# Performance work log

Measured on AMD Instinct MI355X. Metric: run time of the kernel, lower is better.

## Reference

```python
import jax, jax.numpy as jnp
import numpy as np

T, B, IN, H, L = 1024, 32, 512, 512, 2


def setup_inputs() -> dict:
    key = jax.random.key(0)
    ks = jax.random.split(key, 9)
    stdv = 1.0 / np.sqrt(H)
    u = lambda k, shape: jax.random.uniform(k, shape, jnp.float32, -stdv, stdv)
    return {
        "x": jax.random.normal(ks[0], (T, B, IN), jnp.float32),
        "w_ih0": u(ks[1], (4 * H, IN)),
        "w_hh0": u(ks[2], (4 * H, H)),
        "b_ih0": jnp.zeros((4 * H,), jnp.float32),
        "b_hh0": jnp.zeros((4 * H,), jnp.float32),
        "w_ih1": u(ks[3], (4 * H, H)),
        "w_hh1": u(ks[4], (4 * H, H)),
        "b_ih1": jnp.zeros((4 * H,), jnp.float32),
        "b_hh1": jnp.zeros((4 * H,), jnp.float32),
        "h0": jnp.zeros((L, B, H), jnp.float32),
        "c0": jnp.zeros((L, B, H), jnp.float32),
    }


def _lstm_layer(x, w_ih, b_ih, w_hh, b_hh, h0, c0):
    # Precompute input projection for the whole sequence (in2hidden), then
    # scan the strictly sequential hidden recurrence over time.
    gi = jnp.einsum("tbi,gi->tbg", x, w_ih) + b_ih  # (T, B, 4H)

    def step(carry, g):
        h, c = carry
        gates = g + h @ w_hh.T + b_hh  # (B, 4H)
        i, f, gcell, o = jnp.split(gates, 4, axis=-1)
        i = jax.nn.sigmoid(i)
        f = jax.nn.sigmoid(f)
        gcell = jnp.tanh(gcell)
        o = jax.nn.sigmoid(o)
        c = f * c + i * gcell
        h = o * jnp.tanh(c)
        return (h, c), h

    (hT, cT), hs = jax.lax.scan(step, (h0, c0), gi)
    return hs, hT, cT  # (T,B,H), (B,H), (B,H)


def reference(x, w_ih0, w_hh0, b_ih0, b_hh0, w_ih1, w_hh1, b_ih1, b_hh1, h0, c0):
    out0, h0f, c0f = _lstm_layer(x, w_ih0, b_ih0, w_hh0, b_hh0, h0[0], c0[0])
    out1, h1f, c1f = _lstm_layer(out0, w_ih1, b_ih1, w_hh1, b_hh1, h0[1], c0[1])
    h_n = jnp.stack([h0f, h1f])  # (L, B, H)
    c_n = jnp.stack([c0f, c1f])
    return out1, h_n, c_n
```

## Files before the change

### kernel.cpp

```cpp
#include <hip/hip_runtime.h>

#define TT 1024
#define BB 32
#define HH 512

typedef __attribute__((ext_vector_type(8))) __bf16 bf16x8;
typedef __attribute__((ext_vector_type(8))) short short8;
typedef __attribute__((ext_vector_type(4))) float f32x4;

union frag_u {
  short8 s;
  bf16x8 b;
  f32x4 f;
  unsigned long long q[2];
  unsigned int d[4];
};

__device__ __forceinline__ unsigned short f2bf(float f) {
  unsigned int u = __float_as_uint(f);
  u += 0x7FFFu + ((u >> 16) & 1u);
  return (unsigned short)(u >> 16);
}

__device__ __forceinline__ bf16x8 cvt8(const float* p) {
  frag_u u;
#pragma unroll
  for (int j = 0; j < 8; ++j) u.s[j] = (short)f2bf(p[j]);
  return u.b;
}

__device__ __forceinline__ float sigm(float x) {
  return __builtin_amdgcn_rcpf(1.0f + __expf(-x));
}
__device__ __forceinline__ float tanh_(float x) {
  return 1.0f - 2.0f * __builtin_amdgcn_rcpf(1.0f + __expf(2.0f * x));
}

__device__ __forceinline__ void lgkm0() {
  asm volatile("s_waitcnt lgkmcnt(0)" ::: "memory");
}

#define GISSUE16(A0, A1, A2, A3, FR)                                        \
  asm volatile(                                                             \
      "global_load_dwordx4 %0, %16, off sc0 sc1\n\t"                        \
      "global_load_dwordx4 %1, %16, off offset:1024 sc0 sc1\n\t"            \
      "global_load_dwordx4 %2, %16, off offset:2048 sc0 sc1\n\t"            \
      "global_load_dwordx4 %3, %16, off offset:3072 sc0 sc1\n\t"            \
      "global_load_dwordx4 %4, %17, off sc0 sc1\n\t"                        \
      "global_load_dwordx4 %5, %17, off offset:1024 sc0 sc1\n\t"            \
      "global_load_dwordx4 %6, %17, off offset:2048 sc0 sc1\n\t"            \
      "global_load_dwordx4 %7, %17, off offset:3072 sc0 sc1\n\t"            \
      "global_load_dwordx4 %8, %18, off sc0 sc1\n\t"                        \
      "global_load_dwordx4 %9, %18, off offset:1024 sc0 sc1\n\t"            \
      "global_load_dwordx4 %10, %18, off offset:2048 sc0 sc1\n\t"           \
      "global_load_dwordx4 %11, %18, off offset:3072 sc0 sc1\n\t"           \
      "global_load_dwordx4 %12, %19, off sc0 sc1\n\t"                       \
      "global_load_dwordx4 %13, %19, off offset:1024 sc0 sc1\n\t"           \
      "global_load_dwordx4 %14, %19, off offset:2048 sc0 sc1\n\t"           \
      "global_load_dwordx4 %15, %19, off offset:3072 sc0 sc1"               \
      : "=&v"((FR)[0].f), "=&v"((FR)[1].f), "=&v"((FR)[2].f),               \
        "=&v"((FR)[3].f), "=&v"((FR)[4].f), "=&v"((FR)[5].f),               \
        "=&v"((FR)[6].f), "=&v"((FR)[7].f), "=&v"((FR)[8].f),               \
        "=&v"((FR)[9].f), "=&v"((FR)[10].f), "=&v"((FR)[11].f),             \
        "=&v"((FR)[12].f), "=&v"((FR)[13].f), "=&v"((FR)[14].f),            \
        "=&v"((FR)[15].f)                                                   \
      : "v"((A0)), "v"((A1)), "v"((A2)), "v"((A3))                          \
      : "memory")

#define POLLWAIT                                       \
  do {                                                 \
    asm volatile("s_waitcnt vmcnt(0)" ::: "memory");   \
    __builtin_amdgcn_sched_barrier(0);                 \
  } while (0)

__device__ __forceinline__ unsigned int frbad(const frag_u fr[16]) {
  unsigned int bad = 0u;
#pragma unroll
  for (int j = 0; j < 16; ++j)
#pragma unroll
    for (int d = 0; d < 4; ++d) bad |= (fr[j].d[d] == 0xFFFFFFFFu) ? 1u : 0u;
  return bad;
}

__global__ void xcvt(const float* __restrict__ x, unsigned short* __restrict__ xbf) {
  size_t i = (size_t)blockIdx.x * blockDim.x + threadIdx.x;
  const f32x4* p = (const f32x4*)x + 2 * i;
  f32x4 a = p[0], b = p[1];
  short8 o;
  o[0] = (short)f2bf(a[0]); o[1] = (short)f2bf(a[1]);
  o[2] = (short)f2bf(a[2]); o[3] = (short)f2bf(a[3]);
  o[4] = (short)f2bf(b[0]); o[5] = (short)f2bf(b[1]);
  o[6] = (short)f2bf(b[2]); o[7] = (short)f2bf(b[3]);
  *((short8*)xbf + i) = o;
}

__global__ void hfill(unsigned long long* __restrict__ a,
                      unsigned long long* __restrict__ b) {
  size_t base = (size_t)blockIdx.x * 1024 + threadIdx.x;
#pragma unroll
  for (int k = 0; k < 4; ++k) {
    size_t i = base + (size_t)k * 256;
    __hip_atomic_store(a + i, ~0ull, __ATOMIC_RELAXED, __HIP_MEMORY_SCOPE_AGENT);
    __hip_atomic_store(b + i, ~0ull, __ATOMIC_RELAXED, __HIP_MEMORY_SCOPE_AGENT);
  }
}

__global__ __launch_bounds__(64, 1) void lstm_persistent(
    const float* __restrict__ x,
    const float* __restrict__ wih0, const float* __restrict__ whh0,
    const float* __restrict__ bih0, const float* __restrict__ bhh0,
    const float* __restrict__ wih1, const float* __restrict__ whh1,
    const float* __restrict__ bih1, const float* __restrict__ bhh1,
    const float* __restrict__ h0in, const float* __restrict__ c0in,
    float* __restrict__ out,
    const unsigned short* __restrict__ xbf,
    unsigned short* __restrict__ h0buf,
    unsigned short* __restrict__ h1buf)
{
  __shared__ unsigned int xlds[64];

  const int lane = threadIdx.x;
  const int bid = blockIdx.x;
  const int layer = bid >> 7;
  const int sub = bid & 127;
  const int mhalf = sub & 1;
  const int slice = sub >> 1;
  const int hc0 = slice << 3;
  const int q = lane >> 4;
  const int c16 = lane & 15;
  const int cmod = lane & 7;
  const bool owner = (c16 < 8);
  const bool pstore = owner && !(c16 & 1);
  const int mbase = mhalf << 4;

  const float* wih = layer ? wih1 : wih0;
  const float* whh = layer ? whh1 : whh0;
  const float* bih = layer ? bih1 : bih0;
  const float* bhh = layer ? bhh1 : bhh0;

  const int colN0 = owner ? (hc0 + c16) : (512 + hc0 + c16 - 8);
  const int colN1 = owner ? (1024 + hc0 + c16) : (1536 + hc0 + c16 - 8);

  bf16x8 w0[32], w1[32];
#pragma unroll
  for (int kc = 0; kc < 32; ++kc) {
    const float* s0;
    const float* s1;
    if (kc < 16) {
      s0 = wih + (size_t)colN0 * HH + kc * 32 + q * 8;
      s1 = wih + (size_t)colN1 * HH + kc * 32 + q * 8;
    } else {
      s0 = whh + (size_t)colN0 * HH + (kc - 16) * 32 + q * 8;
      s1 = whh + (size_t)colN1 * HH + (kc - 16) * 32 + q * 8;
    }
    w0[kc] = cvt8(s0);
    w1[kc] = cvt8(s1);
  }
  const float bias0 = bih[colN0] + bhh[colN0];
  const float bias1 = bih[colN1] + bhh[colN1];

  float creg[4];
#pragma unroll
  for (int r = 0; r < 4; ++r) {
    int batch = mbase + q * 4 + r;
    creg[r] = c0in[(size_t)layer * BB * HH + (size_t)batch * HH + hc0 + cmod];
  }

  unsigned short* myH = layer ? h1buf : h0buf;
  char* pubbase = (char*)myH + (size_t)mhalf * 16384 + (size_t)slice * 256 +
                  (size_t)lane * 4;

  {
    float hv0[4];
#pragma unroll
    for (int r = 0; r < 4; ++r) {
      int batch = mbase + q * 4 + r;
      hv0[r] = h0in[(size_t)layer * BB * HH + (size_t)batch * HH + hc0 + cmod];
    }
#pragma unroll
    for (int r = 0; r < 4; ++r) {
      unsigned short hb = f2bf(hv0[r]);
      unsigned int partner = (unsigned int)__shfl_xor((int)(unsigned int)hb, 1);
      unsigned int packed = ((unsigned int)hb & 0xffffu) | (partner << 16);
      if (pstore) xlds[(q * 4 + r) * 4 + (cmod >> 1)] = packed;
    }
    lgkm0();
    unsigned int v = xlds[lane];
    __hip_atomic_store((unsigned int*)pubbase, v, __ATOMIC_RELAXED,
                       __HIP_MEMORY_SCOPE_AGENT);
    asm volatile("" ::: "memory");
  }

  const size_t laneoff = (size_t)(mbase + c16) * HH + q * 8;
  const size_t rdlane = (size_t)q * 256 + (size_t)c16 * 16;

  for (int t = 1; t <= TT; ++t) {
    f32x4 acc0 = {bias0, bias0, bias0, bias0};
    f32x4 acc1 = {bias1, bias1, bias1, bias1};

    if (layer == 0) {
      if (xbf != nullptr) {
        const unsigned short* ip = xbf + (size_t)(t - 1) * BB * HH + laneoff;
#pragma unroll
        for (int kc = 0; kc < 16; ++kc) {
          bf16x8 a = *(const bf16x8*)(const void*)(ip + kc * 32);
          acc0 = __builtin_amdgcn_mfma_f32_16x16x32_bf16(a, w0[kc], acc0, 0, 0, 0);
          acc1 = __builtin_amdgcn_mfma_f32_16x16x32_bf16(a, w1[kc], acc1, 0, 0, 0);
        }
      } else {
        const float* ip = x + (size_t)(t - 1) * BB * HH + laneoff;
#pragma unroll
        for (int kc = 0; kc < 16; ++kc) {
          bf16x8 a = cvt8(ip + kc * 32);
          acc0 = __builtin_amdgcn_mfma_f32_16x16x32_bf16(a, w0[kc], acc0, 0, 0, 0);
          acc1 = __builtin_amdgcn_mfma_f32_16x16x32_bf16(a, w1[kc], acc1, 0, 0, 0);
        }
      }

      frag_u fr[16];
      {
        const char* hb = (const char*)myH +
                         ((size_t)(t - 1) * 2 + mhalf) * 16384 + rdlane;
        int it = 0;
        for (;;) {
          ++it;
          GISSUE16(hb, hb + 4096, hb + 8192, hb + 12288, fr);
          POLLWAIT;
          if (__all(frbad(fr) == 0u)) break;
          if (it > (1 << 20)) break;
        }
      }
#pragma unroll
      for (int kc = 0; kc < 16; ++kc) {
        acc0 = __builtin_amdgcn_mfma_f32_16x16x32_bf16(fr[kc].b, w0[16 + kc], acc0, 0, 0, 0);
        acc1 = __builtin_amdgcn_mfma_f32_16x16x32_bf16(fr[kc].b, w1[16 + kc], acc1, 0, 0, 0);
      }
    } else {
      {
        frag_u fb[16];
        const char* hb = (const char*)h1buf +
                         ((size_t)(t - 1) * 2 + mhalf) * 16384 + rdlane;
        int it = 0;
        for (;;) {
          ++it;
          GISSUE16(hb, hb + 4096, hb + 8192, hb + 12288, fb);
          POLLWAIT;
          if (__all(frbad(fb) == 0u)) break;
          if (it > (1 << 20)) break;
        }
#pragma unroll
        for (int kc = 0; kc < 16; ++kc) {
          acc0 = __builtin_amdgcn_mfma_f32_16x16x32_bf16(fb[kc].b, w0[16 + kc], acc0, 0, 0, 0);
          acc1 = __builtin_amdgcn_mfma_f32_16x16x32_bf16(fb[kc].b, w1[16 + kc], acc1, 0, 0, 0);
        }
      }
      {
        frag_u fa[16];
        const char* ha = (const char*)h0buf +
                         ((size_t)t * 2 + mhalf) * 16384 + rdlane;
        int it = 0;
        for (;;) {
          ++it;
          GISSUE16(ha, ha + 4096, ha + 8192, ha + 12288, fa);
          POLLWAIT;
          if (__all(frbad(fa) == 0u)) break;
          if (it > (1 << 20)) break;
        }
#pragma unroll
        for (int kc = 0; kc < 16; ++kc) {
          acc0 = __builtin_amdgcn_mfma_f32_16x16x32_bf16(fa[kc].b, w0[kc], acc0, 0, 0, 0);
          acc1 = __builtin_amdgcn_mfma_f32_16x16x32_bf16(fa[kc].b, w1[kc], acc1, 0, 0, 0);
        }
      }
    }

    float hv[4];
#pragma unroll
    for (int r = 0; r < 4; ++r) {
      float a0 = acc0[r], a1 = acc1[r];
      float p0 = __shfl_xor(a0, 8);
      float p1 = __shfl_xor(a1, 8);
      float iv = owner ? a0 : p0;
      float fv = owner ? p0 : a0;
      float gv = owner ? a1 : p1;
      float ov = owner ? p1 : a1;
      iv = sigm(iv);
      fv = sigm(fv);
      gv = tanh_(gv);
      ov = sigm(ov);
      float cc = fv * creg[r] + iv * gv;
      creg[r] = cc;
      hv[r] = ov * tanh_(cc);
    }

    {
#pragma unroll
      for (int r = 0; r < 4; ++r) {
        unsigned short hb = f2bf(hv[r]);
        unsigned int partner = (unsigned int)__shfl_xor((int)(unsigned int)hb, 1);
        unsigned int packed = ((unsigned int)hb & 0xffffu) | (partner << 16);
        if (pstore) xlds[(q * 4 + r) * 4 + (cmod >> 1)] = packed;
      }
      lgkm0();
      unsigned int v = xlds[lane];
      __hip_atomic_store((unsigned int*)(pubbase + (size_t)t * 32768), v,
                         __ATOMIC_RELAXED, __HIP_MEMORY_SCOPE_AGENT);
      asm volatile("" ::: "memory");
    }

    if (layer) {
      float* op = out + (size_t)(t - 1) * BB * HH;
#pragma unroll
      for (int r = 0; r < 4; ++r) {
        int batch = mbase + q * 4 + r;
        if (owner) op[(size_t)batch * HH + hc0 + cmod] = hv[r];
      }
    }
    if (t == TT) {
      float* hn = out + (size_t)TT * BB * HH + (size_t)layer * BB * HH;
      float* cn = out + (size_t)TT * BB * HH + (size_t)2 * BB * HH + (size_t)layer * BB * HH;
#pragma unroll
      for (int r = 0; r < 4; ++r) {
        int batch = mbase + q * 4 + r;
        if (owner) {
          hn[(size_t)batch * HH + hc0 + cmod] = hv[r];
          cn[(size_t)batch * HH + hc0 + cmod] = creg[r];
        }
      }
    }
  }
}

extern "C" void kernel_launch(void* const* d_in, const int* in_sizes, int n_in,
                              void* d_out, int out_size, void* d_ws, size_t ws_size,
                              hipStream_t stream) {
  (void)in_sizes; (void)n_in; (void)out_size;
  const float* x = (const float*)d_in[0];
  const float* wih0 = (const float*)d_in[1];
  const float* whh0 = (const float*)d_in[2];
  const float* bih0 = (const float*)d_in[3];
  const float* bhh0 = (const float*)d_in[4];
  const float* wih1 = (const float*)d_in[5];
  const float* whh1 = (const float*)d_in[6];
  const float* bih1 = (const float*)d_in[7];
  const float* bhh1 = (const float*)d_in[8];
  const float* h0in = (const float*)d_in[9];
  const float* c0in = (const float*)d_in[10];
  float* out = (float*)d_out;
  char* ws = (char*)d_ws;

  const size_t hbuf_bytes = (size_t)(TT + 1) * 2 * 64 * 256;
  const size_t xbf_bytes = (size_t)TT * BB * HH * 2;

  unsigned short* h0b = (unsigned short*)ws;
  unsigned short* h1b = (unsigned short*)(ws + hbuf_bytes);
  size_t off = 2 * hbuf_bytes;
  bool use_xbf = ws_size >= off + xbf_bytes;
  unsigned short* xbf = use_xbf ? (unsigned short*)(ws + off) : nullptr;

  hfill<<<dim3(4100), dim3(256), 0, stream>>>(
      (unsigned long long*)h0b, (unsigned long long*)h1b);
  if (use_xbf) xcvt<<<dim3(8192), dim3(256), 0, stream>>>(x, xbf);
  lstm_persistent<<<dim3(256), dim3(64), 0, stream>>>(
      x, wih0, whh0, bih0, bhh0, wih1, whh1, bih1, bhh1, h0in, c0in,
      out, xbf, h0b, h1b);
}
```

Baseline: 5.416 ms.

## Prefetch next-step hidden-state and input fragments before polling in recurrent loop

The loads of the next timestep's published hidden-state fragments are now issued right after the current step's h is published. For layer 1 this also covers layer-0's next output, and for layer 0 the bf16 input slice is prefetched into registers a step early. Poll loops first check the speculatively loaded data and reissue loads only if the sentinel is still present, so a full global round-trip should come off the serial critical path. In exchange, register pressure goes up with three 16-fragment arrays held live. For layer 0 the input-projection MFMAs now run after the poll instead of before it, which puts them on the dependency chain.

```diff
diff --git a/kernel.cpp b/kernel.cpp
--- a/kernel.cpp
+++ b/kernel.cpp
@@ -82,6 +82,17 @@
   return bad;
 }
 
+#define POLLLOOP(FR, B0)                                                    \
+  do {                                                                      \
+    int it_ = 0;                                                            \
+    for (;;) {                                                              \
+      POLLWAIT;                                                             \
+      if (__all(frbad(FR) == 0u)) break;                                    \
+      if (++it_ > (1 << 20)) break;                                         \
+      GISSUE16((B0), (B0) + 4096, (B0) + 8192, (B0) + 12288, FR);           \
+    }                                                                       \
+  } while (0)
+
 __global__ void xcvt(const float* __restrict__ x, unsigned short* __restrict__ xbf) {
   size_t i = (size_t)blockIdx.x * blockDim.x + threadIdx.x;
   const f32x4* p = (const f32x4*)x + 2 * i;
@@ -170,6 +181,9 @@
   char* pubbase = (char*)myH + (size_t)mhalf * 16384 + (size_t)slice * 256 +
                   (size_t)lane * 4;
 
+  const size_t laneoff = (size_t)(mbase + c16) * HH + q * 8;
+  const size_t rdlane = (size_t)q * 256 + (size_t)c16 * 16;
+
   {
     float hv0[4];
 #pragma unroll
@@ -191,21 +205,46 @@
     asm volatile("" ::: "memory");
   }
 
-  const size_t laneoff = (size_t)(mbase + c16) * HH + q * 8;
-  const size_t rdlane = (size_t)q * 256 + (size_t)c16 * 16;
+  frag_u fr[16];
+  frag_u fa[16];
+  bf16x8 xa[16];
+
+  const bool use_xa = (layer == 0) && (xbf != nullptr);
+
+  if (layer == 0) {
+    const char* hb = (const char*)myH + (size_t)mhalf * 16384 + rdlane;
+    GISSUE16(hb, hb + 4096, hb + 8192, hb + 12288, fr);
+    if (use_xa) {
+      const unsigned short* ip = xbf + laneoff;
+#pragma unroll
+      for (int kc = 0; kc < 16; ++kc)
+        xa[kc] = *(const bf16x8*)(const void*)(ip + kc * 32);
+    }
+  } else {
+    const char* hb = (const char*)h1buf + (size_t)mhalf * 16384 + rdlane;
+    GISSUE16(hb, hb + 4096, hb + 8192, hb + 12288, fr);
+    const char* ha = (const char*)h0buf + ((size_t)2 + mhalf) * 16384 + rdlane;
+    GISSUE16(ha, ha + 4096, ha + 8192, ha + 12288, fa);
+  }
 
   for (int t = 1; t <= TT; ++t) {
     f32x4 acc0 = {bias0, bias0, bias0, bias0};
     f32x4 acc1 = {bias1, bias1, bias1, bias1};
 
     if (layer == 0) {
-      if (xbf != nullptr) {
-        const unsigned short* ip = xbf + (size_t)(t - 1) * BB * HH + laneoff;
+      const char* hb = (const char*)myH +
+                       ((size_t)(t - 1) * 2 + mhalf) * 16384 + rdlane;
+      POLLLOOP(fr, hb);
+#pragma unroll
+      for (int kc = 0; kc < 16; ++kc) {
+        acc0 = __builtin_amdgcn_mfma_f32_16x16x32_bf16(fr[kc].b, w0[16 + kc], acc0, 0, 0, 0);
+        acc1 = __builtin_amdgcn_mfma_f32_16x16x32_bf16(fr[kc].b, w1[16 + kc], acc1, 0, 0, 0);
+      }
+      if (use_xa) {
 #pragma unroll
         for (int kc = 0; kc < 16; ++kc) {
-          bf16x8 a = *(const bf16x8*)(const void*)(ip + kc * 32);
-          acc0 = __builtin_amdgcn_mfma_f32_16x16x32_bf16(a, w0[kc], acc0, 0, 0, 0);
-          acc1 = __builtin_amdgcn_mfma_f32_16x16x32_bf16(a, w1[kc], acc1, 0, 0, 0);
+          acc0 = __builtin_amdgcn_mfma_f32_16x16x32_bf16(xa[kc], w0[kc], acc0, 0, 0, 0);
+          acc1 = __builtin_amdgcn_mfma_f32_16x16x32_bf16(xa[kc], w1[kc], acc1, 0, 0, 0);
         }
       } else {
         const float* ip = x + (size_t)(t - 1) * BB * HH + laneoff;
@@ -216,61 +255,30 @@
           acc1 = __builtin_amdgcn_mfma_f32_16x16x32_bf16(a, w1[kc], acc1, 0, 0, 0);
         }
       }
-
-      frag_u fr[16];
-      {
-        const char* hb = (const char*)myH +
-                         ((size_t)(t - 1) * 2 + mhalf) * 16384 + rdlane;
-        int it = 0;
-        for (;;) {
-          ++it;
-          GISSUE16(hb, hb + 4096, hb + 8192, hb + 12288, fr);
-          POLLWAIT;
-          if (__all(frbad(fr) == 0u)) break;
-          if (it > (1 << 20)) break;
-        }
-      }
+    } else {
+      const char* hb = (const char*)h1buf +
+                       ((size_t)(t - 1) * 2 + mhalf) * 16384 + rdlane;
+      POLLLOOP(fr, hb);
 #pragma unroll
       for (int kc = 0; kc < 16; ++kc) {
         acc0 = __builtin_amdgcn_mfma_f32_16x16x32_bf16(fr[kc].b, w0[16 + kc], acc0, 0, 0, 0);
         acc1 = __builtin_amdgcn_mfma_f32_16x16x32_bf16(fr[kc].b, w1[16 + kc], acc1, 0, 0, 0);
       }
-    } else {
-      {
-        frag_u fb[16];
-        const char* hb = (const char*)h1buf +
-                         ((size_t)(t - 1) * 2 + mhalf) * 16384 + rdlane;
-        int it = 0;
+      const char* ha = (const char*)h0buf +
+                       ((size_t)t * 2 + mhalf) * 16384 + rdlane;
+      if (!__all(frbad(fa) == 0u)) {
+        int it_ = 0;
         for (;;) {
-          ++it;
-          GISSUE16(hb, hb + 4096, hb + 8192, hb + 12288, fb);
-          POLLWAIT;
-          if (__all(frbad(fb) == 0u)) break;
-          if (it > (1 << 20)) break;
-        }
-#pragma unroll
-        for (int kc = 0; kc < 16; ++kc) {
-          acc0 = __builtin_amdgcn_mfma_f32_16x16x32_bf16(fb[kc].b, w0[16 + kc], acc0, 0, 0, 0);
-          acc1 = __builtin_amdgcn_mfma_f32_16x16x32_bf16(fb[kc].b, w1[16 + kc], acc1, 0, 0, 0);
-        }
-      }
-      {
-        frag_u fa[16];
-        const char* ha = (const char*)h0buf +
-                         ((size_t)t * 2 + mhalf) * 16384 + rdlane;
-        int it = 0;
-        for (;;) {
-          ++it;
           GISSUE16(ha, ha + 4096, ha + 8192, ha + 12288, fa);
           POLLWAIT;
           if (__all(frbad(fa) == 0u)) break;
-          if (it > (1 << 20)) break;
+          if (++it_ > (1 << 20)) break;
         }
-#pragma unroll
-        for (int kc = 0; kc < 16; ++kc) {
-          acc0 = __builtin_amdgcn_mfma_f32_16x16x32_bf16(fa[kc].b, w0[kc], acc0, 0, 0, 0);
-          acc1 = __builtin_amdgcn_mfma_f32_16x16x32_bf16(fa[kc].b, w1[kc], acc1, 0, 0, 0);
-        }
+      }
+#pragma unroll
+      for (int kc = 0; kc < 16; ++kc) {
+        acc0 = __builtin_amdgcn_mfma_f32_16x16x32_bf16(fa[kc].b, w0[kc], acc0, 0, 0, 0);
+        acc1 = __builtin_amdgcn_mfma_f32_16x16x32_bf16(fa[kc].b, w1[kc], acc1, 0, 0, 0);
       }
     }
 
@@ -308,6 +316,21 @@
       asm volatile("" ::: "memory");
     }
 
+    if (t < TT) {
+      if (layer == 0) {
+        const char* hb2 = (const char*)myH +
+                          ((size_t)t * 2 + mhalf) * 16384 + rdlane;
+        GISSUE16(hb2, hb2 + 4096, hb2 + 8192, hb2 + 12288, fr);
+      } else {
+        const char* hb2 = (const char*)h1buf +
+                          ((size_t)t * 2 + mhalf) * 16384 + rdlane;
+        GISSUE16(hb2, hb2 + 4096, hb2 + 8192, hb2 + 12288, fr);
+        const char* ha2 = (const char*)h0buf +
+                          ((size_t)(t + 1) * 2 + mhalf) * 16384 + rdlane;
+        GISSUE16(ha2, ha2 + 4096, ha2 + 8192, ha2 + 12288, fa);
+      }
+    }
+
     if (layer) {
       float* op = out + (size_t)(t - 1) * BB * HH;
 #pragma unroll
@@ -327,6 +350,13 @@
           cn[(size_t)batch * HH + hc0 + cmod] = creg[r];
         }
       }
+    }
+
+    if (use_xa && t < TT) {
+      const unsigned short* ip = xbf + (size_t)t * BB * HH + laneoff;
+#pragma unroll
+      for (int kc = 0; kc < 16; ++kc)
+        xa[kc] = *(const bf16x8*)(const void*)(ip + kc * 32);
     }
   }
 }
```

After: 10.38 ms. 1.92x slower.
